# Kernel tuning notes

Measured on AMD Instinct MI355X. Metric: run time of the kernel, lower is better.

Reference implementation:

```python
import jax, jax.numpy as jnp
import numpy as np

B, T, DM, H, D = 4, 2048, 1024, 16, 64
INNER = H * D


def setup_inputs() -> dict:
    key = jax.random.key(0)
    ks = jax.random.split(key, 8)
    s = 0.02
    x = jax.random.normal(ks[0], (B, T, DM), dtype=jnp.float32)
    state = jnp.zeros((B, H, D, D), dtype=jnp.float32)
    Wq = jax.random.normal(ks[1], (DM, INNER), dtype=jnp.float32) * s
    Wk = jax.random.normal(ks[2], (DM, INNER), dtype=jnp.float32) * s
    Wv = jax.random.normal(ks[3], (DM, INNER), dtype=jnp.float32) * s
    Wa = jax.random.normal(ks[4], (DM, H), dtype=jnp.float32) * s
    ba = jnp.zeros((H,), dtype=jnp.float32)
    Wb = jax.random.normal(ks[5], (DM, H), dtype=jnp.float32) * s
    bb = jnp.zeros((H,), dtype=jnp.float32)  # beta_init=0.5 -> logit(0.5)=0
    Wo = jax.random.normal(ks[6], (INNER, DM), dtype=jnp.float32) * s
    return {"x": x, "state": state, "Wq": Wq, "Wk": Wk, "Wv": Wv,
            "Wa": Wa, "ba": ba, "Wb": Wb, "bb": bb, "Wo": Wo}


def reference(x, state, Wq, Wk, Wv, Wa, ba, Wb, bb, Wo):
    Bb, Tt, _ = x.shape
    Q = (x @ Wq).reshape(Bb, Tt, H, D)
    K = (x @ Wk).reshape(Bb, Tt, H, D)
    V = (x @ Wv).reshape(Bb, Tt, H, D)
    alpha = jax.nn.sigmoid(x @ Wa + ba)  # (B,T,H) forget gate
    beta = jax.nn.sigmoid(x @ Wb + bb)   # (B,T,H) write gate
    # F.normalize(p=2, dim=-1) with eps=1e-12 clamp on the norm
    K = K / jnp.maximum(jnp.linalg.norm(K, axis=-1, keepdims=True), 1e-12)

    def step(S, inp):
        qt, kt, vt, at, bt = inp  # (B,H,D),(B,H,D),(B,H,D),(B,H),(B,H)
        S = at[..., None, None] * S + bt[..., None, None] * jnp.einsum('bhi,bhj->bhij', vt, kt)
        yt = jnp.einsum('bhij,bhj->bhi', S, qt)
        return S, yt

    xs = (jnp.swapaxes(Q, 0, 1), jnp.swapaxes(K, 0, 1), jnp.swapaxes(V, 0, 1),
          jnp.swapaxes(alpha, 0, 1), jnp.swapaxes(beta, 0, 1))
    S, ys = jax.lax.scan(step, state, xs)  # ys: (T,B,H,D)
    out = jnp.swapaxes(ys, 0, 1).reshape(Bb, Tt, INNER) @ Wo
    return out, S
```

## Files before the change

kernel.cpp:

```cpp
#include <hip/hip_runtime.h>
#include <hip/hip_bf16.h>
#include <math.h>

#define B_SZ   4
#define T_LEN  2048
#define DM     1024
#define NH     16
#define DH     64
#define INNER  1024
#define NROWS  (B_SZ*T_LEN)
#define NQ     (NROWS*INNER)
#define CH     64
#define NCH    (T_LEN/CH)

typedef __bf16 bf16x8 __attribute__((ext_vector_type(8)));
typedef __bf16 bf16x4 __attribute__((ext_vector_type(4)));
typedef float  f32x4  __attribute__((ext_vector_type(4)));
typedef __attribute__((address_space(3))) void*       lds_vp;
typedef const __attribute__((address_space(1))) void* gbl_vp;

__device__ __forceinline__ int swz(int row, int col) {
    return (row << 6) + ((((col >> 3) + (row >> 2)) & 7) << 3) + (col & 7);
}

__global__ __launch_bounds__(256) void wt_cast_transpose(const float* __restrict__ Wq,
                                                         const float* __restrict__ Wk,
                                                         const float* __restrict__ Wv,
                                                         const float* __restrict__ Wo,
                                                         __bf16* __restrict__ WqT,
                                                         __bf16* __restrict__ WkT,
                                                         __bf16* __restrict__ WvT,
                                                         __bf16* __restrict__ WoT) {
    __shared__ float tile[64][65];
    const float* W;
    __bf16* WT;
    if      (blockIdx.z == 0) { W = Wq; WT = WqT; }
    else if (blockIdx.z == 1) { W = Wk; WT = WkT; }
    else if (blockIdx.z == 2) { W = Wv; WT = WvT; }
    else                      { W = Wo; WT = WoT; }

    const int k0 = blockIdx.y * 64, n0 = blockIdx.x * 64;
    const int tr  = threadIdx.x >> 4;
    const int tc4 = (threadIdx.x & 15) * 4;

#pragma unroll
    for (int r = 0; r < 4; r++) {
        const int k = tr + 16 * r;
        const float4 v = *(const float4*)(W + (size_t)(k0 + k) * DM + n0 + tc4);
        tile[k][tc4 + 0] = v.x;
        tile[k][tc4 + 1] = v.y;
        tile[k][tc4 + 2] = v.z;
        tile[k][tc4 + 3] = v.w;
    }
    __syncthreads();
#pragma unroll
    for (int r = 0; r < 4; r++) {
        const int n = tr + 16 * r;
        bf16x4 o;
#pragma unroll
        for (int j = 0; j < 4; j++) o[j] = (__bf16)tile[tc4 + j][n];
        *(bf16x4*)(WT + (size_t)(n0 + n) * DM + k0 + tc4) = o;
    }
}

template <typename CT>
__device__ __forceinline__ void gemm_bf16_body(const __bf16* __restrict__ A,
                                               const __bf16* __restrict__ BT,
                                               CT* __restrict__ C,
                                               int Ndim, int Kdim,
                                               int m0, int n0) {
    __shared__ __align__(16) __bf16 lA[128 * 32];
    __shared__ __align__(16) __bf16 lB[128 * 32];

    const int tid  = threadIdx.x;
    const int wid  = tid >> 6;
    const int lane = tid & 63;
    const int wm = (wid >> 1) * 64, wn = (wid & 1) * 64;

    f32x4 acc[4][4];
#pragma unroll
    for (int i = 0; i < 4; i++)
#pragma unroll
        for (int j = 0; j < 4; j++) acc[i][j] = (f32x4)0.f;

    const int srow = wid * 32 + (lane >> 2);
    const int scol = (lane & 3) * 8;
    const __bf16* gA = A  + (size_t)(m0 + srow) * Kdim + scol;
    const __bf16* gB = BT + (size_t)(n0 + srow) * Kdim + scol;

    const int qoff = (lane >> 4) * 8;
    const int frow = lane & 15;

    for (int k0 = 0; k0 < Kdim; k0 += 32) {
        __syncthreads();
#pragma unroll
        for (int i = 0; i < 2; i++) {
            __builtin_amdgcn_global_load_lds((gbl_vp)(gA + k0 + (size_t)i * 16 * Kdim),
                                             (lds_vp)(&lA[(wid * 32 + i * 16) * 32]),
                                             16, 0, 0);
            __builtin_amdgcn_global_load_lds((gbl_vp)(gB + k0 + (size_t)i * 16 * Kdim),
                                             (lds_vp)(&lB[(wid * 32 + i * 16) * 32]),
                                             16, 0, 0);
        }
        __syncthreads();

        bf16x8 af[4], bfr[4];
#pragma unroll
        for (int t = 0; t < 4; t++) {
            af[t]  = *(const bf16x8*)&lA[(wm + t * 16 + frow) * 32 + qoff];
            bfr[t] = *(const bf16x8*)&lB[(wn + t * 16 + frow) * 32 + qoff];
        }
#pragma unroll
        for (int mi = 0; mi < 4; mi++)
#pragma unroll
            for (int nj = 0; nj < 4; nj++)
                acc[mi][nj] = __builtin_amdgcn_mfma_f32_16x16x32_bf16(
                    af[mi], bfr[nj], acc[mi][nj], 0, 0, 0);
    }

    const int cr = (lane >> 4) * 4, cc = lane & 15;
#pragma unroll
    for (int mi = 0; mi < 4; mi++) {
#pragma unroll
        for (int nj = 0; nj < 4; nj++) {
            CT* Cp = C + (size_t)(m0 + wm + mi * 16 + cr) * Ndim + n0 + wn + nj * 16 + cc;
#pragma unroll
            for (int r = 0; r < 4; r++) Cp[(size_t)r * Ndim] = (CT)acc[mi][nj][r];
        }
    }
}

__device__ __forceinline__ void xcd_swz(int& mt, int& nt) {
    const int id = blockIdx.y * gridDim.x + blockIdx.x;
    const int xcd = id & 7, j = id >> 3;
    mt = xcd * 8 + (j >> 3);
    nt = j & 7;
}

__global__ __launch_bounds__(256) void qkv_gemm_bf16(const __bf16* __restrict__ xb,
                                                     const __bf16* __restrict__ WqT,
                                                     const __bf16* __restrict__ WkT,
                                                     const __bf16* __restrict__ WvT,
                                                     __bf16* __restrict__ Q,
                                                     __bf16* __restrict__ K_,
                                                     __bf16* __restrict__ V) {
    const __bf16* BT = (blockIdx.z == 0) ? WqT : ((blockIdx.z == 1) ? WkT : WvT);
    __bf16*       Cm = (blockIdx.z == 0) ? Q   : ((blockIdx.z == 1) ? K_  : V);
    int mt, nt; xcd_swz(mt, nt);
    gemm_bf16_body<__bf16>(xb, BT, Cm, INNER, DM, mt * 128, nt * 128);
}

__global__ __launch_bounds__(256) void out_gemm_bf16(const __bf16* __restrict__ Yb,
                                                     const __bf16* __restrict__ WoT,
                                                     float* __restrict__ Cout) {
    int mt, nt; xcd_swz(mt, nt);
    gemm_bf16_body<float>(Yb, WoT, Cout, DM, INNER, mt * 128, nt * 128);
}

#define WGS 1032
#define LAS 40
__global__ __launch_bounds__(256) void gates_fused(const float* __restrict__ x,
                                                   const float* __restrict__ Wa,
                                                   const float* __restrict__ ba,
                                                   const float* __restrict__ Wb,
                                                   const float* __restrict__ bb,
                                                   float* __restrict__ AlphaT,
                                                   float* __restrict__ BetaT,
                                                   __bf16* __restrict__ xb) {
    __shared__ __align__(16) __bf16 lWg[32 * WGS];
    __shared__ __align__(16) __bf16 lA[64 * LAS];

    const int tid = threadIdx.x;
    const int wid = tid >> 6, lane = tid & 63;
    const int quad = lane >> 4, frow = lane & 15;
    const int m0 = blockIdx.x * 64;

    {
        const int kbase = tid * 4;
#pragma unroll
        for (int j = 0; j < 4; j++) {
            const int k = kbase + j;
            const float4* war = (const float4*)(Wa + (size_t)k * NH);
            const float4* wbr = (const float4*)(Wb + (size_t)k * NH);
#pragma unroll
            for (int q = 0; q < 4; q++) {
                const float4 a = war[q], bq = wbr[q];
                lWg[(q * 4 + 0) * WGS + k] = (__bf16)a.x;
                lWg[(q * 4 + 1) * WGS + k] = (__bf16)a.y;
                lWg[(q * 4 + 2) * WGS + k] = (__bf16)a.z;
                lWg[(q * 4 + 3) * WGS + k] = (__bf16)a.w;
                lWg[(16 + q * 4 + 0) * WGS + k] = (__bf16)bq.x;
                lWg[(16 + q * 4 + 1) * WGS + k] = (__bf16)bq.y;
                lWg[(16 + q * 4 + 2) * WGS + k] = (__bf16)bq.z;
                lWg[(16 + q * 4 + 3) * WGS + k] = (__bf16)bq.w;
            }
        }
    }
    const float bias_a = ba[frow];
    const float bias_b = bb[frow];

    const int rrow = tid >> 2;
    const int rk   = (tid & 3) * 8;
    const float* xrow = x + (size_t)(m0 + rrow) * DM + rk;
    float4 c0 = *(const float4*)(xrow + 0);
    float4 c1 = *(const float4*)(xrow + 4);

    f32x4 acc[2];
    acc[0] = (f32x4)0.f; acc[1] = (f32x4)0.f;

    for (int k0 = 0; k0 < DM; k0 += 32) {
        __syncthreads();
        bf16x8 xv;
        xv[0] = (__bf16)c0.x; xv[1] = (__bf16)c0.y; xv[2] = (__bf16)c0.z; xv[3] = (__bf16)c0.w;
        xv[4] = (__bf16)c1.x; xv[5] = (__bf16)c1.y; xv[6] = (__bf16)c1.z; xv[7] = (__bf16)c1.w;
        *(bf16x8*)&lA[rrow * LAS + rk] = xv;
        *(bf16x8*)(xb + (size_t)(m0 + rrow) * DM + k0 + rk) = xv;
        if (k0 + 32 < DM) {
            c0 = *(const float4*)(xrow + k0 + 32);
            c1 = *(const float4*)(xrow + k0 + 36);
        }
        __syncthreads();
        const bf16x8 af = *(const bf16x8*)&lA[(wid * 16 + frow) * LAS + quad * 8];
#pragma unroll
        for (int ct = 0; ct < 2; ct++) {
            const bf16x8 bf = *(const bf16x8*)&lWg[(ct * 16 + frow) * WGS + k0 + quad * 8];
            acc[ct] = __builtin_amdgcn_mfma_f32_16x16x32_bf16(af, bf, acc[ct], 0, 0, 0);
        }
    }

#pragma unroll
    for (int ct = 0; ct < 2; ct++) {
        const float bias = (ct == 0) ? bias_a : bias_b;
        float* dst = (ct == 0) ? AlphaT : BetaT;
#pragma unroll
        for (int r = 0; r < 4; r++) {
            const int row = m0 + wid * 16 + quad * 4 + r;
            const float s = acc[ct][r] + bias;
            dst[(size_t)frow * NROWS + row] = 1.f / (1.f + __expf(-s));
        }
    }
}

__global__ __launch_bounds__(256) void chunk_ds(const __bf16* __restrict__ Q,
                                                const __bf16* __restrict__ K,
                                                __bf16* __restrict__ V,
                                                const float* __restrict__ AlphaT,
                                                const float* __restrict__ BetaT,
                                                float* __restrict__ Dec,
                                                float* __restrict__ DS,
                                                float* __restrict__ ExpT) {
    __shared__ __align__(16) __bf16 Qb[64 * 64];
    __shared__ __align__(16) __bf16 Kb[64 * 64];
    __shared__ __align__(16) __bf16 KTs[64 * 64];
    __shared__ __align__(16) __bf16 VTb[64 * 64];
    __shared__ __align__(16) __bf16 Ab[64 * 64];
    __shared__ float sla[64], sb[64], swd[64];

    const int blk = blockIdx.x;
    const int c = blk & 31, h = (blk >> 5) & 15, b = blk >> 9;
    const int t0 = c * CH;
    const int tid = threadIdx.x;
    const int wid = tid >> 6, lane = tid & 63;
    const size_t rowbase = ((size_t)(b * T_LEN + t0) * NH + h) * DH;

    const int srow = tid >> 3;
    const int scol = (tid & 7) * 8;
    bf16x8 q8[2], k8[2], v8[2];
#pragma unroll
    for (int r = 0; r < 2; r++) {
        const size_t g = rowbase + (size_t)(srow + 32 * r) * INNER + scol;
        q8[r] = *(const bf16x8*)(Q + g);
        k8[r] = *(const bf16x8*)(K + g);
        v8[r] = *(const bf16x8*)(V + g);
    }

    if (tid < 64) {
        const int t = tid;
        const size_t gaT = (size_t)h * NROWS + b * T_LEN + t0 + t;
        const float a  = AlphaT[gaT];
        const float bt = BetaT[gaT];
        float xx = logf(a);
#pragma unroll
        for (int off = 1; off < 64; off <<= 1) {
            const float y = __shfl_up(xx, off, 64);
            if (t >= off) xx += y;
        }
        const float la63 = __shfl(xx, 63, 64);
        sla[t] = xx;
        sb[t]  = bt;
        swd[t] = bt * __expf(la63 - xx);
        ExpT[gaT] = __expf(xx);
        if (t == 63) Dec[(size_t)(b * NH + h) * NCH + c] = __expf(la63);
    }
    __syncthreads();

#pragma unroll
    for (int r = 0; r < 2; r++) {
        const int row = srow + 32 * r;
        float kf[8];
        float ss = 0.f;
#pragma unroll
        for (int j = 0; j < 8; j++) { kf[j] = (float)k8[r][j]; ss += kf[j] * kf[j]; }
        ss += __shfl_xor(ss, 1, 64);
        ss += __shfl_xor(ss, 2, 64);
        ss += __shfl_xor(ss, 4, 64);
        const float scale = 1.f / fmaxf(sqrtf(ss), 1e-12f);
        const float w = swd[row];
        bf16x8 kn8;
#pragma unroll
        for (int j = 0; j < 8; j++) {
            const float kn = kf[j] * scale;
            kn8[j] = (__bf16)kn;
            KTs[swz(scol + j, row)] = (__bf16)(w * kn);
            VTb[swz(scol + j, row)] = v8[r][j];
        }
        *(bf16x8*)&Qb[swz(row, scol)] = q8[r];
        *(bf16x8*)&Kb[swz(row, scol)] = kn8;
    }
    __syncthreads();

    const int quad = lane >> 4;
    const int frow = lane & 15;
    const int tw = wid * 16;

    f32x4 accG[4];
#pragma unroll
    for (int i = 0; i < 4; i++) accG[i] = (f32x4)0.f;
#pragma unroll
    for (int ks = 0; ks < 2; ks++) {
        const int ko = quad * 8 + 32 * ks;
        const bf16x8 aq = *(const bf16x8*)&Qb[swz(tw + frow, ko)];
#pragma unroll
        for (int st = 0; st < 4; st++) {
            const bf16x8 bk = *(const bf16x8*)&Kb[swz(st * 16 + frow, ko)];
            accG[st] = __builtin_amdgcn_mfma_f32_16x16x32_bf16(aq, bk, accG[st], 0, 0, 0);
        }
    }
#pragma unroll
    for (int st = 0; st < 4; st++) {
#pragma unroll
        for (int r = 0; r < 4; r++) {
            const int t = tw + quad * 4 + r;
            const int s = st * 16 + frow;
            const float av = (s <= t) ? __expf(sla[t] - sla[s]) * sb[s] * accG[st][r] : 0.f;
            Ab[swz(t, s)] = (__bf16)av;
        }
    }
    __syncthreads();

    f32x4 accY[4], accD[4];
#pragma unroll
    for (int i = 0; i < 4; i++) { accY[i] = (f32x4)0.f; accD[i] = (f32x4)0.f; }
#pragma unroll
    for (int ks = 0; ks < 2; ks++) {
        const int ko = quad * 8 + 32 * ks;
        const bf16x8 aA = *(const bf16x8*)&Ab[swz(tw + frow, ko)];
        const bf16x8 aV = *(const bf16x8*)&VTb[swz(tw + frow, ko)];
#pragma unroll
        for (int jt = 0; jt < 4; jt++) {
            const bf16x8 bv = *(const bf16x8*)&VTb[swz(jt * 16 + frow, ko)];
            const bf16x8 bk = *(const bf16x8*)&KTs[swz(jt * 16 + frow, ko)];
            accY[jt] = __builtin_amdgcn_mfma_f32_16x16x32_bf16(aA, bv, accY[jt], 0, 0, 0);
            accD[jt] = __builtin_amdgcn_mfma_f32_16x16x32_bf16(aV, bk, accD[jt], 0, 0, 0);
        }
    }
#pragma unroll
    for (int jt = 0; jt < 4; jt++) {
#pragma unroll
        for (int r = 0; r < 4; r++) {
            const int row = tw + quad * 4 + r;
            const size_t g = rowbase + (size_t)row * INNER + jt * 16 + frow;
            V[g]  = (__bf16)accY[jt][r];
            DS[g] = accD[jt][r];
        }
    }
}

__global__ __launch_bounds__(256) void chunk_state(const float* __restrict__ DS,
                                                   const float* __restrict__ Dec,
                                                   const float* __restrict__ state_in,
                                                   float* __restrict__ state_out,
                                                   __bf16* __restrict__ ScB) {
    const int blk = blockIdx.x;
    const int b = blk >> 4, h = blk & 15;
    const int tid = threadIdx.x;
    const int w = tid >> 6;
    const int l = tid & 63;

    float S[16];
    {
        const float* st = state_in + ((size_t)(b * NH + h) * DH + l) * DH + 16 * w;
#pragma unroll
        for (int j4 = 0; j4 < 4; j4++)
            *(float4*)&S[4 * j4] = *(const float4*)(st + 4 * j4);
    }

    for (int c = 0; c < NCH; c++) {
        const int t0 = c * CH;
        const float decay = Dec[(size_t)(b * NH + h) * NCH + c];
        const size_t off = ((size_t)(b * T_LEN + t0 + l) * NH + h) * DH + 16 * w;
        const float* ds = DS + off;
        __bf16* sc = ScB + off;
        float4 dv[4];
#pragma unroll
        for (int j4 = 0; j4 < 4; j4++) dv[j4] = *(const float4*)(ds + 4 * j4);
#pragma unroll
        for (int j4 = 0; j4 < 4; j4++) {
            bf16x4 o;
            o[0] = (__bf16)S[4 * j4 + 0]; o[1] = (__bf16)S[4 * j4 + 1];
            o[2] = (__bf16)S[4 * j4 + 2]; o[3] = (__bf16)S[4 * j4 + 3];
            *(bf16x4*)(sc + 4 * j4) = o;
        }
#pragma unroll
        for (int j4 = 0; j4 < 4; j4++) {
            S[4 * j4 + 0] = decay * S[4 * j4 + 0] + dv[j4].x;
            S[4 * j4 + 1] = decay * S[4 * j4 + 1] + dv[j4].y;
            S[4 * j4 + 2] = decay * S[4 * j4 + 2] + dv[j4].z;
            S[4 * j4 + 3] = decay * S[4 * j4 + 3] + dv[j4].w;
        }
    }

    float* so = state_out + ((size_t)(b * NH + h) * DH + l) * DH + 16 * w;
#pragma unroll
    for (int j4 = 0; j4 < 4; j4++)
        *(float4*)(so + 4 * j4) = *(const float4*)&S[4 * j4];
}

__global__ __launch_bounds__(256) void chunk_y(const __bf16* __restrict__ Q,
                                               const __bf16* __restrict__ ScB,
                                               __bf16* __restrict__ Yb,
                                               const float* __restrict__ ExpT) {
    __shared__ __align__(16) __bf16 Qb[64 * 64];
    __shared__ __align__(16) __bf16 Scb[64 * 64];
    __shared__ float sexp[64];

    const int blk = blockIdx.x;
    const int c = blk & 31, h = (blk >> 5) & 15, b = blk >> 9;
    const int t0 = c * CH;
    const int tid = threadIdx.x;
    const int wid = tid >> 6, lane = tid & 63;
    const size_t rowbase = ((size_t)(b * T_LEN + t0) * NH + h) * DH;

    const int srow = tid >> 3;
    const int scol = (tid & 7) * 8;
    bf16x8 q8[2], s8[2];
#pragma unroll
    for (int r = 0; r < 2; r++) {
        const size_t g = rowbase + (size_t)(srow + 32 * r) * INNER + scol;
        q8[r] = *(const bf16x8*)(Q + g);
        s8[r] = *(const bf16x8*)(ScB + g);
    }

    if (tid < 64)
        sexp[tid] = ExpT[(size_t)h * NROWS + b * T_LEN + t0 + tid];

#pragma unroll
    for (int r = 0; r < 2; r++) {
        *(bf16x8*)&Qb[swz(srow + 32 * r, scol)]  = q8[r];
        *(bf16x8*)&Scb[swz(srow + 32 * r, scol)] = s8[r];
    }
    __syncthreads();

    const int quad = lane >> 4;
    const int frow = lane & 15;
    const int tw = wid * 16;

    f32x4 accU[4];
#pragma unroll
    for (int i = 0; i < 4; i++) accU[i] = (f32x4)0.f;
#pragma unroll
    for (int ks = 0; ks < 2; ks++) {
        const int ko = quad * 8 + 32 * ks;
        const bf16x8 aq = *(const bf16x8*)&Qb[swz(tw + frow, ko)];
#pragma unroll
        for (int it = 0; it < 4; it++) {
            const bf16x8 bs = *(const bf16x8*)&Scb[swz(it * 16 + frow, ko)];
            accU[it] = __builtin_amdgcn_mfma_f32_16x16x32_bf16(aq, bs, accU[it], 0, 0, 0);
        }
    }

#pragma unroll
    for (int it = 0; it < 4; it++) {
#pragma unroll
        for (int r = 0; r < 4; r++) {
            const int t = tw + quad * 4 + r;
            const size_t g = rowbase + (size_t)t * INNER + it * 16 + frow;
            Yb[g] = (__bf16)(sexp[t] * accU[it][r] + (float)Yb[g]);
        }
    }
}

extern "C" void kernel_launch(void* const* d_in, const int* in_sizes, int n_in,
                              void* d_out, int out_size, void* d_ws, size_t ws_size,
                              hipStream_t stream) {
    const float* x     = (const float*)d_in[0];
    const float* state = (const float*)d_in[1];
    const float* Wq    = (const float*)d_in[2];
    const float* Wk    = (const float*)d_in[3];
    const float* Wv    = (const float*)d_in[4];
    const float* Wa    = (const float*)d_in[5];
    const float* ba    = (const float*)d_in[6];
    const float* Wb    = (const float*)d_in[7];
    const float* bb    = (const float*)d_in[8];
    const float* Wo    = (const float*)d_in[9];

    __bf16* Qb    = (__bf16*)d_ws;
    __bf16* Kbf   = Qb + (size_t)NQ;
    __bf16* Vbf   = Kbf + (size_t)NQ;
    float*  DS    = (float*)(Vbf + (size_t)NQ);
    float*  AlphaT= DS + (size_t)NQ;
    float*  BetaT = AlphaT + (size_t)NROWS * NH;
    float*  ExpT  = BetaT + (size_t)NROWS * NH;
    float*  Dec   = ExpT + (size_t)NROWS * NH;
    __bf16* xb    = (__bf16*)(Dec + (size_t)B_SZ * NH * NCH);
    __bf16* ScB   = xb;
    __bf16* WqT   = xb + (size_t)NQ;
    __bf16* WkT   = WqT + (size_t)DM * INNER;
    __bf16* WvT   = WkT + (size_t)DM * INNER;
    __bf16* WoT   = WvT + (size_t)DM * INNER;

    float* out  = (float*)d_out;
    float* Sout = out + (size_t)NQ;

    wt_cast_transpose<<<dim3(16, 16, 4), 256, 0, stream>>>(Wq, Wk, Wv, Wo,
                                                           WqT, WkT, WvT, WoT);
    gates_fused<<<NROWS / 64, 256, 0, stream>>>(x, Wa, ba, Wb, bb,
                                                AlphaT, BetaT, xb);
    qkv_gemm_bf16<<<dim3(INNER / 128, NROWS / 128, 3), 256, 0, stream>>>(
        xb, WqT, WkT, WvT, Qb, Kbf, Vbf);
    chunk_ds<<<B_SZ * NH * NCH, 256, 0, stream>>>(Qb, Kbf, Vbf, AlphaT, BetaT,
                                                  Dec, DS, ExpT);
    chunk_state<<<B_SZ * NH, 256, 0, stream>>>(DS, Dec, state, Sout, ScB);
    chunk_y<<<B_SZ * NH * NCH, 256, 0, stream>>>(Qb, ScB, Vbf, ExpT);
    out_gemm_bf16<<<dim3(DM / 128, NROWS / 128), 256, 0, stream>>>(Vbf, WoT, out);
}
```

Baseline: 288.3 us.

## Replace bf16 GEMMs with double-buffered 256x128 tile pipelined kernel

Rewrites the QKV and output projection GEMMs as a 512-thread, 256x128-tile kernel. It double-buffers K=64 slabs in 96KB of swizzled LDS and splits each slab into two phases, so global-to-LDS loads for the next slabs overlap the MFMA work. The three QKV projections become one flat launch over concatenated weights, with an XCD-aware block remap and raised wave priority during the MFMA bursts. The goal is to hide memory latency and cut the synchronisation stalls of the single-buffered loop. In exchange it relies on contiguous Q/K/V and weight buffers, hardcodes the 1024 dimensions, and its large LDS footprint limits occupancy.

```diff
diff --git a/kernel.cpp b/kernel.cpp
--- a/kernel.cpp
+++ b/kernel.cpp
@@ -63,19 +63,47 @@
     }
 }
 
+#define A_LOFF(buf_, kh_) ((buf_) * 32768 + (kh_) * 16384)
+#define B_LOFF(buf_, kh_) (65536 + (buf_) * 16384 + (kh_) * 8192)
+
 template <typename CT>
-__device__ __forceinline__ void gemm_bf16_body(const __bf16* __restrict__ A,
-                                               const __bf16* __restrict__ BT,
-                                               CT* __restrict__ C,
-                                               int Ndim, int Kdim,
-                                               int m0, int n0) {
-    __shared__ __align__(16) __bf16 lA[128 * 32];
-    __shared__ __align__(16) __bf16 lB[128 * 32];
+__device__ __forceinline__ void gemm_8ph_body(const __bf16* __restrict__ A,
+                                              const __bf16* __restrict__ BT,
+                                              CT* __restrict__ C,
+                                              int m0, int n0bt, int n0c) {
+    __shared__ __align__(16) char lds[98304];
 
     const int tid  = threadIdx.x;
     const int wid  = tid >> 6;
     const int lane = tid & 63;
-    const int wm = (wid >> 1) * 64, wn = (wid & 1) * 64;
+    const int wm = wid >> 1;
+    const int wn = wid & 1;
+    const int frow = lane & 15, quad = lane >> 4;
+
+    int offA[4], offB[4];
+#pragma unroll
+    for (int i = 0; i < 4; ++i) {
+        const int ra = wm * 64 + i * 16 + frow;
+        offA[i] = ra * 64 + ((quad ^ ((ra >> 1) & 3)) << 4);
+        const int rb = wn * 64 + i * 16 + frow;
+        offB[i] = rb * 64 + ((quad ^ ((rb >> 1) & 3)) << 4);
+    }
+
+    const int lr = lane >> 2;
+    const int cs = ((lane & 3) ^ ((lane >> 3) & 3)) << 3;
+    const __bf16* gA0 = A  + (size_t)(m0 + (wid * 2 + 0) * 16 + lr) * 1024 + cs;
+    const __bf16* gA1 = A  + (size_t)(m0 + (wid * 2 + 1) * 16 + lr) * 1024 + cs;
+    const __bf16* gB  = BT + (size_t)(n0bt + wid * 16 + lr) * 1024 + cs;
+
+#define STG_A(t_, kh_) do {                                                        \
+        __builtin_amdgcn_global_load_lds((gbl_vp)(gA0 + (t_) * 64 + (kh_) * 32),   \
+            (lds_vp)(lds + A_LOFF((t_) & 1, kh_) + (wid * 2 + 0) * 1024), 16, 0, 0); \
+        __builtin_amdgcn_global_load_lds((gbl_vp)(gA1 + (t_) * 64 + (kh_) * 32),   \
+            (lds_vp)(lds + A_LOFF((t_) & 1, kh_) + (wid * 2 + 1) * 1024), 16, 0, 0); \
+    } while (0)
+#define STG_B(t_, kh_)                                                             \
+        __builtin_amdgcn_global_load_lds((gbl_vp)(gB + (t_) * 64 + (kh_) * 32),    \
+            (lds_vp)(lds + B_LOFF((t_) & 1, kh_) + wid * 1024), 16, 0, 0)
 
     f32x4 acc[4][4];
 #pragma unroll
@@ -83,78 +111,82 @@
 #pragma unroll
         for (int j = 0; j < 4; j++) acc[i][j] = (f32x4)0.f;
 
-    const int srow = wid * 32 + (lane >> 2);
-    const int scol = (lane & 3) * 8;
-    const __bf16* gA = A  + (size_t)(m0 + srow) * Kdim + scol;
-    const __bf16* gB = BT + (size_t)(n0 + srow) * Kdim + scol;
-
-    const int qoff = (lane >> 4) * 8;
-    const int frow = lane & 15;
-
-    for (int k0 = 0; k0 < Kdim; k0 += 32) {
-        __syncthreads();
-#pragma unroll
-        for (int i = 0; i < 2; i++) {
-            __builtin_amdgcn_global_load_lds((gbl_vp)(gA + k0 + (size_t)i * 16 * Kdim),
-                                             (lds_vp)(&lA[(wid * 32 + i * 16) * 32]),
-                                             16, 0, 0);
-            __builtin_amdgcn_global_load_lds((gbl_vp)(gB + k0 + (size_t)i * 16 * Kdim),
-                                             (lds_vp)(&lB[(wid * 32 + i * 16) * 32]),
-                                             16, 0, 0);
-        }
-        __syncthreads();
-
-        bf16x8 af[4], bfr[4];
-#pragma unroll
-        for (int t = 0; t < 4; t++) {
-            af[t]  = *(const bf16x8*)&lA[(wm + t * 16 + frow) * 32 + qoff];
-            bfr[t] = *(const bf16x8*)&lB[(wn + t * 16 + frow) * 32 + qoff];
-        }
-#pragma unroll
-        for (int mi = 0; mi < 4; mi++)
-#pragma unroll
-            for (int nj = 0; nj < 4; nj++)
-                acc[mi][nj] = __builtin_amdgcn_mfma_f32_16x16x32_bf16(
-                    af[mi], bfr[nj], acc[mi][nj], 0, 0, 0);
-    }
-
-    const int cr = (lane >> 4) * 4, cc = lane & 15;
-#pragma unroll
-    for (int mi = 0; mi < 4; mi++) {
-#pragma unroll
-        for (int nj = 0; nj < 4; nj++) {
-            CT* Cp = C + (size_t)(m0 + wm + mi * 16 + cr) * Ndim + n0 + wn + nj * 16 + cc;
-#pragma unroll
-            for (int r = 0; r < 4; r++) Cp[(size_t)r * Ndim] = (CT)acc[mi][nj][r];
-        }
-    }
-}
-
-__device__ __forceinline__ void xcd_swz(int& mt, int& nt) {
-    const int id = blockIdx.y * gridDim.x + blockIdx.x;
-    const int xcd = id & 7, j = id >> 3;
-    mt = xcd * 8 + (j >> 3);
-    nt = j & 7;
-}
-
-__global__ __launch_bounds__(256) void qkv_gemm_bf16(const __bf16* __restrict__ xb,
-                                                     const __bf16* __restrict__ WqT,
-                                                     const __bf16* __restrict__ WkT,
-                                                     const __bf16* __restrict__ WvT,
-                                                     __bf16* __restrict__ Q,
-                                                     __bf16* __restrict__ K_,
-                                                     __bf16* __restrict__ V) {
-    const __bf16* BT = (blockIdx.z == 0) ? WqT : ((blockIdx.z == 1) ? WkT : WvT);
-    __bf16*       Cm = (blockIdx.z == 0) ? Q   : ((blockIdx.z == 1) ? K_  : V);
-    int mt, nt; xcd_swz(mt, nt);
-    gemm_bf16_body<__bf16>(xb, BT, Cm, INNER, DM, mt * 128, nt * 128);
-}
-
-__global__ __launch_bounds__(256) void out_gemm_bf16(const __bf16* __restrict__ Yb,
-                                                     const __bf16* __restrict__ WoT,
-                                                     float* __restrict__ Cout) {
-    int mt, nt; xcd_swz(mt, nt);
-    gemm_bf16_body<float>(Yb, WoT, Cout, DM, INNER, mt * 128, nt * 128);
+    STG_A(0, 0); STG_A(0, 1); STG_B(0, 0); STG_B(0, 1);
+    STG_A(1, 0); STG_B(1, 0);
+    asm volatile("s_waitcnt vmcnt(3)" ::: "memory");
+    asm volatile("s_barrier" ::: "memory");
+
+#define PHASE(u_, kh_, STG_STMT, VM_STMT)                                          \
+    {                                                                              \
+        const char* Ab_ = lds + A_LOFF((u_) & 1, kh_);                             \
+        const char* Bb_ = lds + B_LOFF((u_) & 1, kh_);                             \
+        bf16x8 af_[4], bfr_[4];                                                    \
+        _Pragma("unroll")                                                          \
+        for (int i_ = 0; i_ < 4; ++i_) {                                           \
+            af_[i_]  = *(const bf16x8*)(Ab_ + offA[i_]);                           \
+            bfr_[i_] = *(const bf16x8*)(Bb_ + offB[i_]);                           \
+        }                                                                          \
+        STG_STMT;                                                                  \
+        asm volatile("s_barrier" ::: "memory");                                    \
+        asm volatile("s_waitcnt lgkmcnt(0)" ::: "memory");                         \
+        __builtin_amdgcn_sched_barrier(0);                                         \
+        __builtin_amdgcn_s_setprio(1);                                             \
+        _Pragma("unroll")                                                          \
+        for (int mi_ = 0; mi_ < 4; ++mi_)                                          \
+            _Pragma("unroll")                                                      \
+            for (int nj_ = 0; nj_ < 4; ++nj_)                                      \
+                acc[mi_][nj_] = __builtin_amdgcn_mfma_f32_16x16x32_bf16(           \
+                    af_[mi_], bfr_[nj_], acc[mi_][nj_], 0, 0, 0);                  \
+        __builtin_amdgcn_s_setprio(0);                                             \
+        VM_STMT;                                                                   \
+        asm volatile("s_barrier" ::: "memory");                                    \
+    }
+
+    for (int u = 0; u < 14; ++u) {
+        PHASE(u, 0, { STG_A(u + 1, 1); STG_B(u + 1, 1); }, );
+        PHASE(u, 1, { STG_A(u + 2, 0); STG_B(u + 2, 0); },
+              asm volatile("s_waitcnt vmcnt(3)" ::: "memory"));
+    }
+    PHASE(14, 0, { STG_A(15, 1); STG_B(15, 1); }, );
+    PHASE(14, 1, { }, asm volatile("s_waitcnt vmcnt(0)" ::: "memory"));
+    PHASE(15, 0, { }, );
+    PHASE(15, 1, { }, );
+
+#undef PHASE
+#undef STG_A
+#undef STG_B
+
+    const int cr = quad * 4, cc = frow;
+#pragma unroll
+    for (int mi = 0; mi < 4; ++mi) {
+#pragma unroll
+        for (int nj = 0; nj < 4; ++nj) {
+            CT* Cp = C + (size_t)(m0 + wm * 64 + mi * 16 + cr) * 1024
+                       + n0c + wn * 64 + nj * 16 + cc;
+#pragma unroll
+            for (int r = 0; r < 4; r++) Cp[(size_t)r * 1024] = (CT)acc[mi][nj][r];
+        }
+    }
+}
+
+__global__ __launch_bounds__(512, 2) void qkv_gemm_8ph(const __bf16* __restrict__ xb,
+                                                       const __bf16* __restrict__ BTall,
+                                                       __bf16* __restrict__ QKV) {
+    const int id = blockIdx.x;
+    const int wg = (id & 7) * 96 + (id >> 3);
+    const int mt = wg / 24, nt = wg % 24;
+    const int mat = nt >> 3;
+    gemm_8ph_body<__bf16>(xb, BTall, QKV + (size_t)mat * NQ,
+                          mt * 256, nt * 128, (nt & 7) * 128);
+}
+
+__global__ __launch_bounds__(512, 2) void out_gemm_8ph(const __bf16* __restrict__ Yb,
+                                                       const __bf16* __restrict__ WoT,
+                                                       float* __restrict__ Cout) {
+    const int id = blockIdx.x;
+    const int wg = (id & 7) * 32 + (id >> 3);
+    const int mt = wg >> 3, nt = wg & 7;
+    gemm_8ph_body<float>(Yb, WoT, Cout, mt * 256, nt * 128, nt * 128);
 }
 
 #define WGS 1032
@@ -526,11 +558,10 @@
                                                            WqT, WkT, WvT, WoT);
     gates_fused<<<NROWS / 64, 256, 0, stream>>>(x, Wa, ba, Wb, bb,
                                                 AlphaT, BetaT, xb);
-    qkv_gemm_bf16<<<dim3(INNER / 128, NROWS / 128, 3), 256, 0, stream>>>(
-        xb, WqT, WkT, WvT, Qb, Kbf, Vbf);
+    qkv_gemm_8ph<<<768, 512, 0, stream>>>(xb, WqT, Qb);
     chunk_ds<<<B_SZ * NH * NCH, 256, 0, stream>>>(Qb, Kbf, Vbf, AlphaT, BetaT,
                                                   Dec, DS, ExpT);
     chunk_state<<<B_SZ * NH, 256, 0, stream>>>(DS, Dec, state, Sout, ScB);
     chunk_y<<<B_SZ * NH * NCH, 256, 0, stream>>>(Qb, ScB, Vbf, ExpT);
-    out_gemm_bf16<<<dim3(DM / 128, NROWS / 128), 256, 0, stream>>>(Vbf, WoT, out);
-}
+    out_gemm_8ph<<<256, 512, 0, stream>>>(Vbf, WoT, out);
+}
```

Measured after the change: 292.2 us. Within noise of the previous version (+1.3%).
